# Kernel tuning notes

Measured on AMD Instinct MI355X. Metric: run time of the kernel, lower is better.

## Reference

```python
import jax, jax.numpy as jnp
import numpy as np

N_ENT = 100000
K = 64
D = 500            # emb_dim (complex half-dim); entity embedding is 2*D
R = 237            # num_relations
ATTN = 128
B = 1024
ETA_MAX = 0.5


def setup_inputs() -> dict:
    key = jax.random.key(0)
    ks = jax.random.split(key, 12)
    anchor_ids = jax.random.randint(ks[0], (B,), 0, N_ENT)
    nbr_ent = jax.random.randint(ks[1], (N_ENT, K), 0, N_ENT)
    nbr_rel = jax.random.randint(ks[2], (N_ENT, K), 0, R)
    nbr_dir = jax.random.randint(ks[3], (N_ENT, K), 0, 2).astype(bool)
    nbr_mask = jax.random.randint(ks[4], (N_ENT, K), 0, 2).astype(bool)
    freq = jax.random.uniform(ks[5], (N_ENT,), dtype=jnp.float32) * 1000.0
    entity_embedding = jax.random.normal(ks[6], (N_ENT, 2 * D), dtype=jnp.float32) * 0.1
    # relation phases; get_relation_reim -> (cos(phase), sin(phase))
    rel_phase = jax.random.uniform(ks[7], (R, D), dtype=jnp.float32, minval=-np.pi, maxval=np.pi)
    a_param = jnp.ones((D,), dtype=jnp.float32)
    eta_raw = jnp.float32(-6.0)
    w_raw = jnp.float32(1.0)
    b = jnp.float32(0.0)
    Wq = jax.random.normal(ks[8], (ATTN, 2 * D), dtype=jnp.float32) * 0.01
    Wk = jax.random.normal(ks[9], (ATTN, 2 * D), dtype=jnp.float32) * 0.01
    rel_bias = jax.random.normal(ks[10], (R, 1), dtype=jnp.float32) * 0.01
    dir_bias = jax.random.normal(ks[11], (2, 1), dtype=jnp.float32) * 0.01
    return dict(anchor_ids=anchor_ids, nbr_ent=nbr_ent, nbr_rel=nbr_rel,
                nbr_dir=nbr_dir, nbr_mask=nbr_mask, freq=freq,
                entity_embedding=entity_embedding, rel_phase=rel_phase,
                a_param=a_param, eta_raw=eta_raw, w_raw=w_raw, b=b,
                Wq=Wq, Wk=Wk, rel_bias=rel_bias, dir_bias=dir_bias)


def reference(anchor_ids, nbr_ent, nbr_rel, nbr_dir, nbr_mask, freq,
              entity_embedding, rel_phase, a_param, eta_raw, w_raw, b,
              Wq, Wk, rel_bias, dir_bias):
    # gather per-anchor neighbor tables: [B, K]
    a_ent = nbr_ent[anchor_ids]
    a_rel = nbr_rel[anchor_ids]
    a_dir = nbr_dir[anchor_ids]
    a_msk = nbr_mask[anchor_ids]

    # neighbor entity embeddings [B, K, 2D] -> complex halves [B, K, D]
    e_j = entity_embedding[a_ent]
    re_j, im_j = jnp.split(e_j, 2, axis=-1)

    # RotatE relation rotation (conjugate when dir==True)
    phase = rel_phase[a_rel]                      # [B, K, D]
    re_r = jnp.cos(phase)
    im_r = jnp.sin(phase)
    im_sel = jnp.where(a_dir[..., None], -im_r, im_r)
    re_msg = re_j * re_r - im_j * im_sel
    im_msg = re_j * im_sel + im_j * re_r
    hat = jnp.concatenate([re_msg, im_msg], axis=-1)  # [B, K, 2D]

    e_i = entity_embedding[anchor_ids]            # [B, 2D]

    # small QK attention with relation/direction bias
    q = e_i @ Wq.T                                # [B, A]
    k = hat @ Wk.T                                # [B, K, A]
    scale = max(ATTN ** 0.5, 1e-6)
    logits = jnp.einsum('ba,bka->bk', q, k) / scale
    dir_id = a_dir.astype(jnp.int32)
    logits = logits + rel_bias[a_rel][..., 0] + dir_bias[dir_id][..., 0]
    logits = jnp.where(a_msk, logits, -10000.0)

    has_nbr = jnp.any(a_msk, axis=1)              # [B]
    logits = jnp.where(has_nbr[:, None], logits, 0.0)
    attn = jax.nn.softmax(logits, axis=1)
    attn = jnp.where(has_nbr[:, None], attn, 0.0)

    delta = jnp.einsum('bk,bkd->bd', attn, hat)   # [B, 2D]
    delta = jnp.where(has_nbr[:, None], delta, e_i)

    # frequency-gated interpolation
    logf = jnp.log1p(freq[anchor_ids])
    w = jax.nn.softplus(w_raw)
    eta = ETA_MAX * jax.nn.sigmoid(eta_raw + w * (-logf) + b)
    eta = eta * has_nbr.astype(eta.dtype)

    re_d, im_d = jnp.split(delta, 2, axis=-1)
    re_d = a_param * re_d
    im_d = a_param * im_d
    re_i, im_i = jnp.split(e_i, 2, axis=-1)
    re_out = re_i + eta[:, None] * (re_d - re_i)
    im_out = im_i + eta[:, None] * (im_d - im_i)
    return jnp.concatenate([re_out, im_out], axis=-1)
```

## Files before the change

### kernel.cpp

```cpp
#include <hip/hip_runtime.h>
#include <math.h>

#define N_ENT 100000
#define KNBR 64
#define DHALF 500
#define TWO_D 1000
#define ATTN_DIM 128
#define ETA_MAX 0.5f

__global__ __launch_bounds__(256) void precompute_m(
    const int* __restrict__ anchor_ids,
    const float* __restrict__ E,
    const float* __restrict__ Wq,
    const float* __restrict__ Wk,
    float* __restrict__ M, int B)
{
    __shared__ float e_lds[8][TWO_D];
    __shared__ float qp[2][8][ATTN_DIM];
    __shared__ float q_lds[8][ATTN_DIM];
    const int t  = threadIdx.x;
    const int b0 = blockIdx.x * 8;

    for (int j = 0; j < 8; ++j) {
        int bb = b0 + j;
        int row = (bb < B) ? anchor_ids[bb] : 0;
        if (t < 250) {
            const float4* src = (const float4*)(E + (size_t)row * TWO_D);
            float4 v = src[t];
            e_lds[j][4 * t + 0] = v.x;
            e_lds[j][4 * t + 1] = v.y;
            e_lds[j][4 * t + 2] = v.z;
            e_lds[j][4 * t + 3] = v.w;
        }
    }
    __syncthreads();

    {
        const int a = t & 127;
        const int h = t >> 7;
        float acc[8] = {0.f, 0.f, 0.f, 0.f, 0.f, 0.f, 0.f, 0.f};
        const float* wrow = Wq + (size_t)a * TWO_D + h * DHALF;
        for (int d = 0; d < DHALF; ++d) {
            float w = wrow[d];
            int dd = h * DHALF + d;
#pragma unroll
            for (int j = 0; j < 8; ++j) acc[j] += w * e_lds[j][dd];
        }
#pragma unroll
        for (int j = 0; j < 8; ++j) qp[h][j][a] = acc[j];
    }
    __syncthreads();
    for (int idx = t; idx < 8 * ATTN_DIM; idx += 256) {
        ((float*)q_lds)[idx] = ((float*)qp)[idx] + ((float*)qp)[8 * ATTN_DIM + idx];
    }
    __syncthreads();

    const float inv_scale = 0.0883883476483184f;
    float acc2[4][8];
#pragma unroll
    for (int c = 0; c < 4; ++c)
#pragma unroll
        for (int j = 0; j < 8; ++j) acc2[c][j] = 0.f;

    for (int a = 0; a < ATTN_DIM; ++a) {
        const float* wkrow = Wk + (size_t)a * TWO_D;
        float wk[4];
#pragma unroll
        for (int c = 0; c < 4; ++c) {
            int d = t + 256 * c;
            wk[c] = (d < TWO_D) ? wkrow[d] : 0.f;
        }
#pragma unroll
        for (int j = 0; j < 8; ++j) {
            float qv = q_lds[j][a];
#pragma unroll
            for (int c = 0; c < 4; ++c) acc2[c][j] += qv * wk[c];
        }
    }
#pragma unroll
    for (int c = 0; c < 4; ++c) {
        int d = t + 256 * c;
        if (d < TWO_D) {
#pragma unroll
            for (int j = 0; j < 8; ++j) {
                int bb = b0 + j;
                if (bb < B) M[(size_t)bb * TWO_D + d] = acc2[c][j] * inv_scale;
            }
        }
    }
}

__global__ __launch_bounds__(256) void refine(
    const int* __restrict__ anchor_ids,
    const int* __restrict__ nbr_ent,
    const int* __restrict__ nbr_rel,
    const int* __restrict__ nbr_dir,
    const int* __restrict__ nbr_mask,
    const float* __restrict__ freq,
    const float* __restrict__ E,
    const float* __restrict__ P,
    const float* __restrict__ a_param,
    const float* __restrict__ eta_raw_p,
    const float* __restrict__ w_raw_p,
    const float* __restrict__ b_p,
    const float* __restrict__ rel_bias,
    const float* __restrict__ dir_bias,
    const float* __restrict__ M,
    float* __restrict__ out)
{
    __shared__ float m_lds[TWO_D];
    __shared__ float accm[4][TWO_D];
    __shared__ float sum_s[4];
    __shared__ int ent_s[KNBR], rel_s[KNBR], dir_s[KNBR], msk_s[KNBR];

    const int t = threadIdx.x;
    const int bid = blockIdx.x;
    const int anchor = anchor_ids[bid];

    for (int idx = t; idx < TWO_D; idx += 256)
        m_lds[idx] = M[(size_t)bid * TWO_D + idx];
    if (t < KNBR) {
        size_t off = (size_t)anchor * KNBR + t;
        ent_s[t] = nbr_ent[off];
        rel_s[t] = nbr_rel[off];
        dir_s[t] = nbr_dir[off];
        msk_s[t] = nbr_mask[off];
    }
    __syncthreads();

    const int lane = t & 63;
    const int wid = t >> 6;

    float mre[8], mim[8];
#pragma unroll
    for (int i = 0; i < 8; ++i) {
        int d = lane + 64 * i;
        mre[i] = (d < DHALF) ? m_lds[d] : 0.f;
        mim[i] = (d < DHALF) ? m_lds[DHALF + d] : 0.f;
    }

    float accre[8], accim[8];
#pragma unroll
    for (int i = 0; i < 8; ++i) { accre[i] = 0.f; accim[i] = 0.f; }
    float wsum = 0.f;
    const float db0 = dir_bias[0];
    const float db1 = dir_bias[1];

    for (int k = wid; k < KNBR; k += 4) {
        if (!msk_s[k]) continue;
        const int ent = ent_s[k];
        const int rel = rel_s[k];
        const int dirf = dir_s[k];
        const float* erow = E + (size_t)ent * TWO_D;
        const float* prow = P + (size_t)rel * DHALF;

        float hre[8], him[8];
        float dot = 0.f;
#pragma unroll
        for (int i = 0; i < 8; ++i) {
            int d = lane + 64 * i;
            if (d < DHALF) {
                float re = erow[d];
                float im = erow[DHALF + d];
                float ph = prow[d];
                float s, c;
                __sincosf(ph, &s, &c);
                if (dirf) s = -s;
                hre[i] = re * c - im * s;
                him[i] = re * s + im * c;
                dot += mre[i] * hre[i] + mim[i] * him[i];
            } else {
                hre[i] = 0.f;
                him[i] = 0.f;
            }
        }
        dot += __shfl_xor(dot, 32);
        dot += __shfl_xor(dot, 16);
        dot += __shfl_xor(dot, 8);
        dot += __shfl_xor(dot, 4);
        dot += __shfl_xor(dot, 2);
        dot += __shfl_xor(dot, 1);

        float logit = dot + rel_bias[rel] + (dirf ? db1 : db0);
        float p = __expf(logit);
        wsum += p;
#pragma unroll
        for (int i = 0; i < 8; ++i) {
            accre[i] += p * hre[i];
            accim[i] += p * him[i];
        }
    }

    if (lane == 0) sum_s[wid] = wsum;
#pragma unroll
    for (int i = 0; i < 8; ++i) {
        int d = lane + 64 * i;
        if (d < DHALF) {
            accm[wid][d] = accre[i];
            accm[wid][DHALF + d] = accim[i];
        }
    }
    __syncthreads();

    const float S = sum_s[0] + sum_s[1] + sum_s[2] + sum_s[3];
    const float invS = (S > 0.f) ? 1.f / S : 0.f;
    float eta = 0.f;
    if (S > 0.f) {
        float logf_ = log1pf(freq[anchor]);
        float wv = log1pf(__expf(w_raw_p[0]));
        float x = eta_raw_p[0] - wv * logf_ + b_p[0];
        eta = ETA_MAX / (1.f + __expf(-x));
    }

    const float* eirow = E + (size_t)anchor * TWO_D;
#pragma unroll
    for (int c = 0; c < 4; ++c) {
        int dd = t + 256 * c;
        if (dd < TWO_D) {
            float delta = (accm[0][dd] + accm[1][dd] + accm[2][dd] + accm[3][dd]) * invS;
            float ei = eirow[dd];
            float ap = a_param[(dd < DHALF) ? dd : dd - DHALF];
            out[(size_t)bid * TWO_D + dd] = ei + eta * (ap * delta - ei);
        }
    }
}

extern "C" void kernel_launch(void* const* d_in, const int* in_sizes, int n_in,
                              void* d_out, int out_size, void* d_ws, size_t ws_size,
                              hipStream_t stream)
{
    const int*   anchor_ids = (const int*)d_in[0];
    const int*   nbr_ent    = (const int*)d_in[1];
    const int*   nbr_rel    = (const int*)d_in[2];
    const int*   nbr_dir    = (const int*)d_in[3];
    const int*   nbr_mask   = (const int*)d_in[4];
    const float* freq       = (const float*)d_in[5];
    const float* E          = (const float*)d_in[6];
    const float* P          = (const float*)d_in[7];
    const float* a_param    = (const float*)d_in[8];
    const float* eta_raw    = (const float*)d_in[9];
    const float* w_raw      = (const float*)d_in[10];
    const float* b_scalar   = (const float*)d_in[11];
    const float* Wq         = (const float*)d_in[12];
    const float* Wk         = (const float*)d_in[13];
    const float* rel_bias   = (const float*)d_in[14];
    const float* dir_bias   = (const float*)d_in[15];
    float* out = (float*)d_out;

    const int B = in_sizes[0];
    float* M = (float*)d_ws;

    precompute_m<<<(B + 7) / 8, 256, 0, stream>>>(anchor_ids, E, Wq, Wk, M, B);
    refine<<<B, 256, 0, stream>>>(anchor_ids, nbr_ent, nbr_rel, nbr_dir, nbr_mask,
                                  freq, E, P, a_param, eta_raw, w_raw, b_scalar,
                                  rel_bias, dir_bias, M, out);
}
```

Baseline: 626.7 us.

## Precompute relation cos/sin table, compact masked neighbors, vectorize and double-buffer gathers

Adds a kernel that builds an interleaved cos/sin table for all relation phases once per call, so refine reads precomputed trig instead of computing sincos per neighbor. Refine now compacts masked neighbors with a ballot into a list, uses float4 loads for embeddings, M and the output, and software-pipelines the neighbor loads across two register buffers. precompute_m processes four anchors per block instead of eight to launch more blocks. The extra trig table doubles the bytes read for the relation rows, and the double buffering raises register pressure under the new occupancy hint.

```diff
diff --git a/kernel.cpp b/kernel.cpp
--- a/kernel.cpp
+++ b/kernel.cpp
@@ -6,7 +6,20 @@
 #define DHALF 500
 #define TWO_D 1000
 #define ATTN_DIM 128
+#define NREL 237
 #define ETA_MAX 0.5f
+
+__global__ __launch_bounds__(256) void build_trig(
+    const float* __restrict__ P, float* __restrict__ CS)
+{
+    int idx = blockIdx.x * 256 + threadIdx.x;
+    if (idx < NREL * DHALF) {
+        float s, c;
+        sincosf(P[idx], &s, &c);
+        CS[2 * idx]     = c;
+        CS[2 * idx + 1] = s;
+    }
+}
 
 __global__ __launch_bounds__(256) void precompute_m(
     const int* __restrict__ anchor_ids,
@@ -15,22 +28,18 @@
     const float* __restrict__ Wk,
     float* __restrict__ M, int B)
 {
-    __shared__ float e_lds[8][TWO_D];
-    __shared__ float qp[2][8][ATTN_DIM];
-    __shared__ float q_lds[8][ATTN_DIM];
+    __shared__ float e_lds[4][TWO_D];
+    __shared__ float qp[2][4][ATTN_DIM];
+    __shared__ float q_lds[4][ATTN_DIM];
     const int t  = threadIdx.x;
-    const int b0 = blockIdx.x * 8;
-
-    for (int j = 0; j < 8; ++j) {
+    const int b0 = blockIdx.x * 4;
+
+    for (int j = 0; j < 4; ++j) {
         int bb = b0 + j;
         int row = (bb < B) ? anchor_ids[bb] : 0;
         if (t < 250) {
-            const float4* src = (const float4*)(E + (size_t)row * TWO_D);
-            float4 v = src[t];
-            e_lds[j][4 * t + 0] = v.x;
-            e_lds[j][4 * t + 1] = v.y;
-            e_lds[j][4 * t + 2] = v.z;
-            e_lds[j][4 * t + 3] = v.w;
+            float4 v = ((const float4*)(E + (size_t)row * TWO_D))[t];
+            ((float4*)&e_lds[j][0])[t] = v;
         }
     }
     __syncthreads();
@@ -38,29 +47,29 @@
     {
         const int a = t & 127;
         const int h = t >> 7;
-        float acc[8] = {0.f, 0.f, 0.f, 0.f, 0.f, 0.f, 0.f, 0.f};
+        float acc[4] = {0.f, 0.f, 0.f, 0.f};
         const float* wrow = Wq + (size_t)a * TWO_D + h * DHALF;
+        const int base = h * DHALF;
         for (int d = 0; d < DHALF; ++d) {
             float w = wrow[d];
-            int dd = h * DHALF + d;
-#pragma unroll
-            for (int j = 0; j < 8; ++j) acc[j] += w * e_lds[j][dd];
-        }
-#pragma unroll
-        for (int j = 0; j < 8; ++j) qp[h][j][a] = acc[j];
-    }
-    __syncthreads();
-    for (int idx = t; idx < 8 * ATTN_DIM; idx += 256) {
-        ((float*)q_lds)[idx] = ((float*)qp)[idx] + ((float*)qp)[8 * ATTN_DIM + idx];
-    }
+            int dd = base + d;
+#pragma unroll
+            for (int j = 0; j < 4; ++j) acc[j] += w * e_lds[j][dd];
+        }
+#pragma unroll
+        for (int j = 0; j < 4; ++j) qp[h][j][a] = acc[j];
+    }
+    __syncthreads();
+    for (int idx = t; idx < 4 * ATTN_DIM; idx += 256)
+        ((float*)q_lds)[idx] = ((float*)qp)[idx] + ((float*)qp)[4 * ATTN_DIM + idx];
     __syncthreads();
 
     const float inv_scale = 0.0883883476483184f;
-    float acc2[4][8];
+    float acc2[4][4];
 #pragma unroll
     for (int c = 0; c < 4; ++c)
 #pragma unroll
-        for (int j = 0; j < 8; ++j) acc2[c][j] = 0.f;
+        for (int j = 0; j < 4; ++j) acc2[c][j] = 0.f;
 
     for (int a = 0; a < ATTN_DIM; ++a) {
         const float* wkrow = Wk + (size_t)a * TWO_D;
@@ -71,7 +80,7 @@
             wk[c] = (d < TWO_D) ? wkrow[d] : 0.f;
         }
 #pragma unroll
-        for (int j = 0; j < 8; ++j) {
+        for (int j = 0; j < 4; ++j) {
             float qv = q_lds[j][a];
 #pragma unroll
             for (int c = 0; c < 4; ++c) acc2[c][j] += qv * wk[c];
@@ -82,7 +91,7 @@
         int d = t + 256 * c;
         if (d < TWO_D) {
 #pragma unroll
-            for (int j = 0; j < 8; ++j) {
+            for (int j = 0; j < 4; ++j) {
                 int bb = b0 + j;
                 if (bb < B) M[(size_t)bb * TWO_D + d] = acc2[c][j] * inv_scale;
             }
@@ -90,7 +99,7 @@
     }
 }
 
-__global__ __launch_bounds__(256) void refine(
+__global__ __launch_bounds__(256, 4) void refine(
     const int* __restrict__ anchor_ids,
     const int* __restrict__ nbr_ent,
     const int* __restrict__ nbr_rel,
@@ -98,7 +107,7 @@
     const int* __restrict__ nbr_mask,
     const float* __restrict__ freq,
     const float* __restrict__ E,
-    const float* __restrict__ P,
+    const float* __restrict__ CS,
     const float* __restrict__ a_param,
     const float* __restrict__ eta_raw_p,
     const float* __restrict__ w_raw_p,
@@ -108,71 +117,89 @@
     const float* __restrict__ M,
     float* __restrict__ out)
 {
-    __shared__ float m_lds[TWO_D];
     __shared__ float accm[4][TWO_D];
     __shared__ float sum_s[4];
-    __shared__ int ent_s[KNBR], rel_s[KNBR], dir_s[KNBR], msk_s[KNBR];
+    __shared__ int ent_s[KNBR], rel_s[KNBR], dir_s[KNBR], list_s[KNBR];
+    __shared__ int cnt_s;
 
     const int t = threadIdx.x;
     const int bid = blockIdx.x;
     const int anchor = anchor_ids[bid];
-
-    for (int idx = t; idx < TWO_D; idx += 256)
-        m_lds[idx] = M[(size_t)bid * TWO_D + idx];
+    const int lane = t & 63;
+    const int wid = t >> 6;
+    const int l1 = (lane < 61) ? lane : 60;
+
     if (t < KNBR) {
         size_t off = (size_t)anchor * KNBR + t;
-        ent_s[t] = nbr_ent[off];
-        rel_s[t] = nbr_rel[off];
-        dir_s[t] = nbr_dir[off];
-        msk_s[t] = nbr_mask[off];
-    }
-    __syncthreads();
-
-    const int lane = t & 63;
-    const int wid = t >> 6;
-
-    float mre[8], mim[8];
-#pragma unroll
-    for (int i = 0; i < 8; ++i) {
-        int d = lane + 64 * i;
-        mre[i] = (d < DHALF) ? m_lds[d] : 0.f;
-        mim[i] = (d < DHALF) ? m_lds[DHALF + d] : 0.f;
-    }
+        int e = nbr_ent[off];
+        int r = nbr_rel[off];
+        int d = nbr_dir[off];
+        int m = nbr_mask[off];
+        ent_s[t] = e; rel_s[t] = r; dir_s[t] = d;
+        unsigned long long bal = __ballot(m != 0);
+        if (m) list_s[__popcll(bal & ((1ull << t) - 1))] = t;
+        if (t == 0) cnt_s = __popcll(bal);
+    }
+
+    const float4* Mr = (const float4*)(M + (size_t)bid * TWO_D);
+    float4 mre0 = Mr[lane];
+    float4 mim0 = Mr[125 + lane];
+    float4 mre1 = Mr[64 + l1];
+    float4 mim1 = Mr[189 + l1];
+    if (lane >= 61) {
+        mre1 = make_float4(0.f, 0.f, 0.f, 0.f);
+        mim1 = make_float4(0.f, 0.f, 0.f, 0.f);
+    }
+    float mreA[8] = {mre0.x, mre0.y, mre0.z, mre0.w, mre1.x, mre1.y, mre1.z, mre1.w};
+    float mimA[8] = {mim0.x, mim0.y, mim0.z, mim0.w, mim1.x, mim1.y, mim1.z, mim1.w};
 
     float accre[8], accim[8];
 #pragma unroll
-    for (int i = 0; i < 8; ++i) { accre[i] = 0.f; accim[i] = 0.f; }
+    for (int q = 0; q < 8; ++q) { accre[q] = 0.f; accim[q] = 0.f; }
     float wsum = 0.f;
     const float db0 = dir_bias[0];
     const float db1 = dir_bias[1];
 
-    for (int k = wid; k < KNBR; k += 4) {
-        if (!msk_s[k]) continue;
-        const int ent = ent_s[k];
-        const int rel = rel_s[k];
-        const int dirf = dir_s[k];
-        const float* erow = E + (size_t)ent * TWO_D;
-        const float* prow = P + (size_t)rel * DHALF;
-
+    __syncthreads();
+    const int n = cnt_s;
+
+    struct NB {
+        float4 re0, im0, re1, im1;
+        float4 csA, csB, csC, csD;
+        float bias, sgn;
+    };
+    NB A, Bq;
+
+    auto load_nb = [&](NB& nb, int slot) {
+        int k = list_s[slot];
+        int df = dir_s[k];
+        const float4* er = (const float4*)(E + (size_t)ent_s[k] * TWO_D);
+        const float4* cr = (const float4*)(CS + (size_t)rel_s[k] * TWO_D);
+        nb.re0 = er[lane];          nb.im0 = er[125 + lane];
+        nb.re1 = er[64 + l1];       nb.im1 = er[189 + l1];
+        nb.csA = cr[2 * lane];      nb.csB = cr[2 * lane + 1];
+        nb.csC = cr[128 + 2 * l1];  nb.csD = cr[129 + 2 * l1];
+        nb.bias = rel_bias[rel_s[k]] + (df ? db1 : db0);
+        nb.sgn = df ? -1.f : 1.f;
+    };
+
+    auto compute_nb = [&](const NB& nb) {
+        float re_[8] = {nb.re0.x, nb.re0.y, nb.re0.z, nb.re0.w,
+                        nb.re1.x, nb.re1.y, nb.re1.z, nb.re1.w};
+        float im_[8] = {nb.im0.x, nb.im0.y, nb.im0.z, nb.im0.w,
+                        nb.im1.x, nb.im1.y, nb.im1.z, nb.im1.w};
+        float cc[8]  = {nb.csA.x, nb.csA.z, nb.csB.x, nb.csB.z,
+                        nb.csC.x, nb.csC.z, nb.csD.x, nb.csD.z};
+        float ssv[8] = {nb.csA.y, nb.csA.w, nb.csB.y, nb.csB.w,
+                        nb.csC.y, nb.csC.w, nb.csD.y, nb.csD.w};
         float hre[8], him[8];
         float dot = 0.f;
 #pragma unroll
-        for (int i = 0; i < 8; ++i) {
-            int d = lane + 64 * i;
-            if (d < DHALF) {
-                float re = erow[d];
-                float im = erow[DHALF + d];
-                float ph = prow[d];
-                float s, c;
-                __sincosf(ph, &s, &c);
-                if (dirf) s = -s;
-                hre[i] = re * c - im * s;
-                him[i] = re * s + im * c;
-                dot += mre[i] * hre[i] + mim[i] * him[i];
-            } else {
-                hre[i] = 0.f;
-                him[i] = 0.f;
-            }
+        for (int q = 0; q < 8; ++q) {
+            float sv = ssv[q] * nb.sgn;
+            hre[q] = re_[q] * cc[q] - im_[q] * sv;
+            him[q] = re_[q] * sv + im_[q] * cc[q];
+            dot += mreA[q] * hre[q] + mimA[q] * him[q];
         }
         dot += __shfl_xor(dot, 32);
         dot += __shfl_xor(dot, 16);
@@ -180,24 +207,41 @@
         dot += __shfl_xor(dot, 4);
         dot += __shfl_xor(dot, 2);
         dot += __shfl_xor(dot, 1);
-
-        float logit = dot + rel_bias[rel] + (dirf ? db1 : db0);
-        float p = __expf(logit);
+        float p = __expf(dot + nb.bias);
         wsum += p;
 #pragma unroll
-        for (int i = 0; i < 8; ++i) {
-            accre[i] += p * hre[i];
-            accim[i] += p * him[i];
+        for (int q = 0; q < 8; ++q) {
+            accre[q] += p * hre[q];
+            accim[q] += p * him[q];
+        }
+    };
+
+    {
+        int i = wid;
+        bool haveA = (i < n);
+        if (haveA) load_nb(A, i);
+        while (haveA) {
+            int iB = i + 4;
+            bool haveB = (iB < n);
+            if (haveB) load_nb(Bq, iB);
+            compute_nb(A);
+            if (!haveB) break;
+            int iA = iB + 4;
+            haveA = (iA < n);
+            if (haveA) load_nb(A, iA);
+            compute_nb(Bq);
+            i = iA;
         }
     }
 
     if (lane == 0) sum_s[wid] = wsum;
-#pragma unroll
-    for (int i = 0; i < 8; ++i) {
-        int d = lane + 64 * i;
-        if (d < DHALF) {
-            accm[wid][d] = accre[i];
-            accm[wid][DHALF + d] = accim[i];
+    {
+        float4* arow = (float4*)&accm[wid][0];
+        arow[lane]       = make_float4(accre[0], accre[1], accre[2], accre[3]);
+        arow[125 + lane] = make_float4(accim[0], accim[1], accim[2], accim[3]);
+        if (lane < 61) {
+            arow[64 + lane]  = make_float4(accre[4], accre[5], accre[6], accre[7]);
+            arow[189 + lane] = make_float4(accim[4], accim[5], accim[6], accim[7]);
         }
     }
     __syncthreads();
@@ -212,16 +256,26 @@
         eta = ETA_MAX / (1.f + __expf(-x));
     }
 
-    const float* eirow = E + (size_t)anchor * TWO_D;
-#pragma unroll
-    for (int c = 0; c < 4; ++c) {
-        int dd = t + 256 * c;
-        if (dd < TWO_D) {
-            float delta = (accm[0][dd] + accm[1][dd] + accm[2][dd] + accm[3][dd]) * invS;
-            float ei = eirow[dd];
-            float ap = a_param[(dd < DHALF) ? dd : dd - DHALF];
-            out[(size_t)bid * TWO_D + dd] = ei + eta * (ap * delta - ei);
-        }
+    if (t < 250) {
+        const float4* r0 = (const float4*)&accm[0][0];
+        const float4* r1 = (const float4*)&accm[1][0];
+        const float4* r2 = (const float4*)&accm[2][0];
+        const float4* r3 = (const float4*)&accm[3][0];
+        float4 a0 = r0[t], a1 = r1[t], a2 = r2[t], a3 = r3[t];
+        float4 delta;
+        delta.x = (a0.x + a1.x + a2.x + a3.x) * invS;
+        delta.y = (a0.y + a1.y + a2.y + a3.y) * invS;
+        delta.z = (a0.z + a1.z + a2.z + a3.z) * invS;
+        delta.w = (a0.w + a1.w + a2.w + a3.w) * invS;
+        const float4* A4 = (const float4*)a_param;
+        float4 ap = (t < 125) ? A4[t] : A4[t - 125];
+        float4 ei = ((const float4*)(E + (size_t)anchor * TWO_D))[t];
+        float4 o;
+        o.x = ei.x + eta * (ap.x * delta.x - ei.x);
+        o.y = ei.y + eta * (ap.y * delta.y - ei.y);
+        o.z = ei.z + eta * (ap.z * delta.z - ei.z);
+        o.w = ei.w + eta * (ap.w * delta.w - ei.w);
+        ((float4*)(out + (size_t)bid * TWO_D))[t] = o;
     }
 }
 
@@ -248,10 +302,12 @@
     float* out = (float*)d_out;
 
     const int B = in_sizes[0];
-    float* M = (float*)d_ws;
-
-    precompute_m<<<(B + 7) / 8, 256, 0, stream>>>(anchor_ids, E, Wq, Wk, M, B);
+    float* M  = (float*)d_ws;
+    float* CS = M + (size_t)B * TWO_D;
+
+    build_trig<<<(NREL * DHALF + 255) / 256, 256, 0, stream>>>(P, CS);
+    precompute_m<<<(B + 3) / 4, 256, 0, stream>>>(anchor_ids, E, Wq, Wk, M, B);
     refine<<<B, 256, 0, stream>>>(anchor_ids, nbr_ent, nbr_rel, nbr_dir, nbr_mask,
-                                  freq, E, P, a_param, eta_raw, w_raw, b_scalar,
+                                  freq, E, CS, a_param, eta_raw, w_raw, b_scalar,
                                   rel_bias, dir_bias, M, out);
 }
```

Result: no change. 626.2 us (-0.1%).
